# Optimization experiments

Hardware: AMD Instinct MI355X
Metric: run time of the kernel (lower is better)

## Reference

```python
import jax, jax.numpy as jnp
import numpy as np

NUM_ITERS = 15
EPSILON = 0.05
MESH_ITERS = 3


def _cost_proj(x, W1, b1, W2, b2):
    # Linear -> ReLU -> Linear
    h = jax.nn.relu(x @ W1 + b1)
    return h @ W2 + b2


def setup_inputs() -> dict:
    key = jax.random.key(0)
    ks = jax.random.split(key, 4)
    B, K, M, D = 8192, 32, 32, 256
    s = 1.0 / np.sqrt(D)
    return {
        "slots_q": jax.random.normal(ks[0], (B, K, D), dtype=jnp.float32),
        "slots_r": jax.random.normal(ks[1], (B, M, D), dtype=jnp.float32),
        "W1": (jax.random.normal(ks[2], (D, D), dtype=jnp.float32) * s),
        "b1": jnp.zeros((D,), dtype=jnp.float32),
        "W2": (jax.random.normal(ks[3], (D, D), dtype=jnp.float32) * s),
        "b2": jnp.zeros((D,), dtype=jnp.float32),
    }


def reference(slots_q, slots_r, W1, b1, W2, b2):
    q = _cost_proj(slots_q, W1, b1, W2, b2)  # [B,K,D]
    r = _cost_proj(slots_r, W1, b1, W2, b2)  # [B,M,D]
    # torch.cdist p=2: pairwise euclidean distance
    sq = (jnp.sum(q * q, -1)[:, :, None]
          + jnp.sum(r * r, -1)[:, None, :]
          - 2.0 * jnp.einsum('bkd,bmd->bkm', q, r))
    C = jnp.sqrt(jnp.clip(sq, 0.0))  # [B,K,M]
    B, K, M = C.shape
    log_K = -C / EPSILON
    log_a = jnp.zeros((B, K, 1), dtype=C.dtype)
    log_b = jnp.zeros((B, 1, M), dtype=C.dtype)
    for _ in range(NUM_ITERS):
        log_a = -jax.nn.logsumexp(log_K + log_b, axis=2, keepdims=True)
        log_b = -jax.nn.logsumexp(log_K + log_a, axis=1, keepdims=True)
    T = jnp.exp(log_K + log_a + log_b)
    for _ in range(MESH_ITERS):
        T = T ** 2
        T = T / (jnp.sum(T, axis=-1, keepdims=True) + 1e-8)
        T = T / (jnp.sum(T, axis=-2, keepdims=True) + 1e-8)
    cost = jnp.sum(T * C, axis=(-1, -2))  # [B]
    similarity = jax.nn.sigmoid(-cost)
    return similarity, T, C, cost
```

## Files before the change

kernel.cpp:

```cpp
#include <hip/hip_runtime.h>
#include <hip/hip_bf16.h>


typedef unsigned short u16;
typedef short short8 __attribute__((ext_vector_type(8)));
typedef float f32x4  __attribute__((ext_vector_type(4)));

#define MFMA(a, b, c) __builtin_amdgcn_mfma_f32_16x16x32_bf16((a), (b), (c), 0, 0, 0)

static __device__ __forceinline__ u16 f2bf(float f) {
  __hip_bfloat16 h = __float2bfloat16(f);
  return __builtin_bit_cast(u16, h);
}
static __device__ __forceinline__ float bf2f(u16 h) {
  return __uint_as_float(((unsigned)h) << 16);
}

__global__ __launch_bounds__(256) void prep_w(const float* __restrict__ W1,
                                              const float* __restrict__ W2,
                                              u16* __restrict__ ws) {
  int id = blockIdx.x * 256 + threadIdx.x;
  int mat = id >> 16;
  int e = id & 65535;
  int k = e >> 8, n = e & 255;
  float wv = (mat ? W2 : W1)[e];
  int ki = k >> 5, kl = k & 31;
  int g = kl >> 3, j = kl & 7;
  int lane = g * 16 + (n & 15);
  int ctg = n >> 4;
  ws[mat * 65536 + ((((ki * 16 + ctg) * 64 + lane) << 3) | j)] = f2bf(wv);
}

struct __align__(16) SMemA {
  u16 F[16384];
  float nrm[64];
};

static __device__ __forceinline__ void gemm_frag(const u16* __restrict__ Af,
                                                 const u16* __restrict__ wf,
                                                 int w, int lane, f32x4 acc[4][2]) {
#pragma unroll
  for (int rt = 0; rt < 4; ++rt) {
    acc[rt][0] = f32x4{0.f, 0.f, 0.f, 0.f};
    acc[rt][1] = f32x4{0.f, 0.f, 0.f, 0.f};
  }
  __builtin_amdgcn_s_setprio(1);
#pragma unroll
  for (int ki = 0; ki < 8; ++ki) {
    const u16* bp = wf + (((ki * 16 + 2 * w) * 64 + lane) << 3);
    short8 b0 = *reinterpret_cast<const short8*>(bp);
    short8 b1 = *reinterpret_cast<const short8*>(bp + 512);
    short8 a[4];
#pragma unroll
    for (int rt = 0; rt < 4; ++rt)
      a[rt] = *reinterpret_cast<const short8*>(Af + (((ki * 4 + rt) * 64 + lane) << 3));
#pragma unroll
    for (int rt = 0; rt < 4; ++rt) {
      acc[rt][0] = MFMA(a[rt], b0, acc[rt][0]);
      acc[rt][1] = MFMA(a[rt], b1, acc[rt][1]);
    }
  }
  __builtin_amdgcn_s_setprio(0);
}

__global__ __launch_bounds__(512, 6) void gemm_cdist(
    const float* __restrict__ slots_q, const float* __restrict__ slots_r,
    const float* __restrict__ b1, const float* __restrict__ b2,
    const u16* __restrict__ ws, float* __restrict__ CO) {
  __shared__ SMemA sm;
  const int tid = threadIdx.x, b = blockIdx.x;
  const int w = tid >> 6, lane = tid & 63, g = lane >> 4, ln = lane & 15;

  {
    const float* srcq = slots_q + (size_t)b * 8192;
    const float* srcr = slots_r + (size_t)b * 8192;
#pragma unroll
    for (int ii = 0; ii < 4; ++ii) {
      int s = tid + ii * 512;
      int ki = s >> 8, rt = (s >> 6) & 3, sg = (s >> 4) & 3, sln = s & 15;
      int row = rt * 16 + sln;
      const float* src = (row < 32) ? (srcq + row * 256) : (srcr + (row - 32) * 256);
      int k0 = ki * 32 + sg * 8;
      float4 v0 = *reinterpret_cast<const float4*>(src + k0);
      float4 v1 = *reinterpret_cast<const float4*>(src + k0 + 4);
      short8 o;
      o[0] = (short)f2bf(v0.x); o[1] = (short)f2bf(v0.y);
      o[2] = (short)f2bf(v0.z); o[3] = (short)f2bf(v0.w);
      o[4] = (short)f2bf(v1.x); o[5] = (short)f2bf(v1.y);
      o[6] = (short)f2bf(v1.z); o[7] = (short)f2bf(v1.w);
      *reinterpret_cast<short8*>(&sm.F[s << 3]) = o;
    }
  }
  float bv1a = b1[32 * w + ln], bv1b = b1[32 * w + 16 + ln];
  float bv2a = b2[32 * w + ln], bv2b = b2[32 * w + 16 + ln];
  __syncthreads();

  f32x4 acc[4][2];
  gemm_frag(sm.F, ws, w, lane, acc);
  __syncthreads();
#pragma unroll
  for (int ct = 0; ct < 2; ++ct) {
    float bv = ct ? bv1b : bv1a;
#pragma unroll
    for (int rt = 0; rt < 4; ++rt)
#pragma unroll
      for (int ri = 0; ri < 4; ++ri) {
        int lane2 = (2 * ct + (ln >> 3)) * 16 + 4 * g + ri;
        sm.F[(((w * 4 + rt) * 64 + lane2) << 3) | (ln & 7)] =
            f2bf(fmaxf(acc[rt][ct][ri] + bv, 0.0f));
      }
  }
  __syncthreads();

  gemm_frag(sm.F, ws + 65536, w, lane, acc);
  __syncthreads();
#pragma unroll
  for (int ct = 0; ct < 2; ++ct) {
    float bv = ct ? bv2b : bv2a;
#pragma unroll
    for (int rt = 0; rt < 4; ++rt)
#pragma unroll
      for (int ri = 0; ri < 4; ++ri) {
        int lane2 = (2 * ct + (ln >> 3)) * 16 + 4 * g + ri;
        sm.F[(((w * 4 + rt) * 64 + lane2) << 3) | (ln & 7)] =
            f2bf(acc[rt][ct][ri] + bv);
      }
  }
  __syncthreads();

  f32x4 dacc = f32x4{0.f, 0.f, 0.f, 0.f};
  if (w < 4) {
    const int mt = w >> 1, nt = w & 1;
    __builtin_amdgcn_s_setprio(1);
#pragma unroll
    for (int ki = 0; ki < 8; ++ki) {
      short8 aq = *reinterpret_cast<const short8*>(
          &sm.F[(((ki * 4 + mt) * 64 + lane) << 3)]);
      short8 br = *reinterpret_cast<const short8*>(
          &sm.F[(((ki * 4 + 2 + nt) * 64 + lane) << 3)]);
      dacc = MFMA(aq, br, dacc);
    }
    __builtin_amdgcn_s_setprio(0);
  } else {
    const int t = w - 4;
    float s = 0.f;
#pragma unroll
    for (int ki = 0; ki < 8; ++ki) {
      short8 v = *reinterpret_cast<const short8*>(
          &sm.F[(((ki * 4 + t) * 64 + lane) << 3)]);
#pragma unroll
      for (int i = 0; i < 8; ++i) {
        float f = bf2f((u16)v[i]);
        s = fmaf(f, f, s);
      }
    }
    s += __shfl_xor(s, 16);
    s += __shfl_xor(s, 32);
    if (lane < 16) sm.nrm[t * 16 + lane] = s;
  }
  __syncthreads();

  if (w < 4) {
    const int mt = w >> 1, nt = w & 1;
    float* Cp = CO + (size_t)b * 1024;
#pragma unroll
    for (int ri = 0; ri < 4; ++ri) {
      int k = mt * 16 + 4 * g + ri;
      int m = nt * 16 + ln;
      float sq = sm.nrm[k] + sm.nrm[32 + m] - 2.0f * dacc[ri];
      Cp[k * 32 + m] = sqrtf(fmaxf(sq, 0.0f));
    }
  }
}

__global__ __launch_bounds__(256, 4) void sinkhorn_mesh(
    const float* __restrict__ CO, float* __restrict__ simO,
    float* __restrict__ TO, float* __restrict__ costO, int Bn) {
  __shared__ float Wl[4][32 * 33];
  __shared__ float ABl[4][64];
  const int wv = threadIdx.x >> 6, lane = threadIdx.x & 63;
  const int p = blockIdx.x * 4 + wv;
  if (p >= Bn) return;
  const int h = lane >> 5, q = lane & 31;
  float* Wm = Wl[wv];
  float* LA = ABl[wv];
  float* LB = ABl[wv] + 32;
  const float* Cp = CO + (size_t)p * 1024;

  float lkr[16], lkc[16];
#pragma unroll
  for (int jj = 0; jj < 4; ++jj) {
    float4 v = *reinterpret_cast<const float4*>(Cp + q * 32 + h * 16 + jj * 4);
    int base = q * 33 + h * 16 + jj * 4;
    Wm[base + 0] = v.x; Wm[base + 1] = v.y; Wm[base + 2] = v.z; Wm[base + 3] = v.w;
    lkr[jj * 4 + 0] = -20.f * v.x; lkr[jj * 4 + 1] = -20.f * v.y;
    lkr[jj * 4 + 2] = -20.f * v.z; lkr[jj * 4 + 3] = -20.f * v.w;
  }
  LB[q] = 0.0f;
  __builtin_amdgcn_wave_barrier();
#pragma unroll
  for (int j = 0; j < 16; ++j) lkc[j] = -20.f * Wm[(h * 16 + j) * 33 + q];

  for (int it = 0; it < 15; ++it) {
    float v[16], mx, s;
#pragma unroll
    for (int j = 0; j < 16; ++j) v[j] = lkr[j] + LB[h * 16 + j];
    mx = v[0];
#pragma unroll
    for (int j = 1; j < 16; ++j) mx = fmaxf(mx, v[j]);
    mx = fmaxf(mx, __shfl_xor(mx, 32));
    s = 0.f;
#pragma unroll
    for (int j = 0; j < 16; ++j) s += __expf(v[j] - mx);
    s += __shfl_xor(s, 32);
    LA[q] = -(mx + __logf(s));
    __builtin_amdgcn_wave_barrier();
#pragma unroll
    for (int j = 0; j < 16; ++j) v[j] = lkc[j] + LA[h * 16 + j];
    mx = v[0];
#pragma unroll
    for (int j = 1; j < 16; ++j) mx = fmaxf(mx, v[j]);
    mx = fmaxf(mx, __shfl_xor(mx, 32));
    s = 0.f;
#pragma unroll
    for (int j = 0; j < 16; ++j) s += __expf(v[j] - mx);
    s += __shfl_xor(s, 32);
    LB[q] = -(mx + __logf(s));
    __builtin_amdgcn_wave_barrier();
  }

  float t[16];
  {
    float la = LA[q];
#pragma unroll
    for (int j = 0; j < 16; ++j) t[j] = __expf(lkr[j] + la + LB[h * 16 + j]);
  }

  for (int mi = 0; mi < 3; ++mi) {
    float s = 0.f;
#pragma unroll
    for (int j = 0; j < 16; ++j) { t[j] *= t[j]; s += t[j]; }
    s += __shfl_xor(s, 32);
    float inv = 1.0f / (s + 1e-8f);
#pragma unroll
    for (int j = 0; j < 16; ++j) Wm[q * 33 + h * 16 + j] = t[j] * inv;
    __builtin_amdgcn_wave_barrier();
#pragma unroll
    for (int j = 0; j < 16; ++j) t[j] = Wm[(h * 16 + j) * 33 + q];
    s = 0.f;
#pragma unroll
    for (int j = 0; j < 16; ++j) s += t[j];
    s += __shfl_xor(s, 32);
    inv = 1.0f / (s + 1e-8f);
#pragma unroll
    for (int j = 0; j < 16; ++j) Wm[(h * 16 + j) * 33 + q] = t[j] * inv;
    __builtin_amdgcn_wave_barrier();
#pragma unroll
    for (int j = 0; j < 16; ++j) t[j] = Wm[q * 33 + h * 16 + j];
  }

  float pp = 0.f;
#pragma unroll
  for (int j = 0; j < 16; ++j) pp = fmaf(t[j], -0.05f * lkr[j], pp);
  pp += __shfl_xor(pp, 1); pp += __shfl_xor(pp, 2); pp += __shfl_xor(pp, 4);
  pp += __shfl_xor(pp, 8); pp += __shfl_xor(pp, 16); pp += __shfl_xor(pp, 32);
  if (lane == 0) {
    costO[p] = pp;
    simO[p] = 1.0f / (1.0f + __expf(pp));
  }
#pragma unroll
  for (int jj = 0; jj < 4; ++jj) {
    float4 o;
    o.x = t[jj * 4 + 0]; o.y = t[jj * 4 + 1];
    o.z = t[jj * 4 + 2]; o.w = t[jj * 4 + 3];
    *reinterpret_cast<float4*>(TO + (size_t)p * 1024 + q * 32 + h * 16 + jj * 4) = o;
  }
}

extern "C" void kernel_launch(void* const* d_in, const int* in_sizes, int n_in,
                              void* d_out, int out_size, void* d_ws, size_t ws_size,
                              hipStream_t stream) {
  const float* slots_q = (const float*)d_in[0];
  const float* slots_r = (const float*)d_in[1];
  const float* W1 = (const float*)d_in[2];
  const float* b1 = (const float*)d_in[3];
  const float* W2 = (const float*)d_in[4];
  const float* b2 = (const float*)d_in[5];
  float* out = (float*)d_out;

  const int Bn = in_sizes[0] / 8192;
  u16* ws = (u16*)d_ws;

  prep_w<<<dim3(512), dim3(256), 0, stream>>>(W1, W2, ws);

  float* simO = out;
  float* TO = out + Bn;
  float* CO = TO + (size_t)Bn * 1024;
  float* costO = CO + (size_t)Bn * 1024;

  gemm_cdist<<<dim3(Bn), dim3(512), 0, stream>>>(slots_q, slots_r, b1, b2, ws, CO);
  sinkhorn_mesh<<<dim3((Bn + 3) / 4), dim3(256), 0, stream>>>(CO, simO, TO, costO, Bn);
}
```

Before: 264.3 us.

## Fuse Sinkhorn and mesh stage into the GEMM/cdist kernel via shared memory

```diff
diff --git a/kernel.cpp b/kernel.cpp
--- a/kernel.cpp
+++ b/kernel.cpp
@@ -63,10 +63,12 @@
   __builtin_amdgcn_s_setprio(0);
 }
 
-__global__ __launch_bounds__(512, 6) void gemm_cdist(
+__global__ __launch_bounds__(512, 8) void gemm_sink(
     const float* __restrict__ slots_q, const float* __restrict__ slots_r,
     const float* __restrict__ b1, const float* __restrict__ b2,
-    const u16* __restrict__ ws, float* __restrict__ CO) {
+    const u16* __restrict__ ws, float* __restrict__ simO,
+    float* __restrict__ TO, float* __restrict__ CO,
+    float* __restrict__ costO) {
   __shared__ SMemA sm;
   const int tid = threadIdx.x, b = blockIdx.x;
   const int w = tid >> 6, lane = tid & 63, g = lane >> 4, ln = lane & 15;
@@ -160,6 +162,8 @@
   }
   __syncthreads();
 
+  float* Cm = reinterpret_cast<float*>(sm.F);
+  float* Wm = Cm + 1056;
   if (w < 4) {
     const int mt = w >> 1, nt = w & 1;
     float* Cp = CO + (size_t)b * 1024;
@@ -168,38 +172,22 @@
       int k = mt * 16 + 4 * g + ri;
       int m = nt * 16 + ln;
       float sq = sm.nrm[k] + sm.nrm[32 + m] - 2.0f * dacc[ri];
-      Cp[k * 32 + m] = sqrtf(fmaxf(sq, 0.0f));
-    }
-  }
-}
-
-__global__ __launch_bounds__(256, 4) void sinkhorn_mesh(
-    const float* __restrict__ CO, float* __restrict__ simO,
-    float* __restrict__ TO, float* __restrict__ costO, int Bn) {
-  __shared__ float Wl[4][32 * 33];
-  __shared__ float ABl[4][64];
-  const int wv = threadIdx.x >> 6, lane = threadIdx.x & 63;
-  const int p = blockIdx.x * 4 + wv;
-  if (p >= Bn) return;
+      float c = sqrtf(fmaxf(sq, 0.0f));
+      Cp[k * 32 + m] = c;
+      Cm[k * 33 + m] = c;
+    }
+  }
+  __syncthreads();
+  if (w != 0) return;
+
   const int h = lane >> 5, q = lane & 31;
-  float* Wm = Wl[wv];
-  float* LA = ABl[wv];
-  float* LB = ABl[wv] + 32;
-  const float* Cp = CO + (size_t)p * 1024;
-
-  float lkr[16], lkc[16];
-#pragma unroll
-  for (int jj = 0; jj < 4; ++jj) {
-    float4 v = *reinterpret_cast<const float4*>(Cp + q * 32 + h * 16 + jj * 4);
-    int base = q * 33 + h * 16 + jj * 4;
-    Wm[base + 0] = v.x; Wm[base + 1] = v.y; Wm[base + 2] = v.z; Wm[base + 3] = v.w;
-    lkr[jj * 4 + 0] = -20.f * v.x; lkr[jj * 4 + 1] = -20.f * v.y;
-    lkr[jj * 4 + 2] = -20.f * v.z; lkr[jj * 4 + 3] = -20.f * v.w;
-  }
-  LB[q] = 0.0f;
+  float* LA = sm.nrm;
+  float* LB = sm.nrm + 32;
+  float lkr[16];
+#pragma unroll
+  for (int j = 0; j < 16; ++j) lkr[j] = -20.f * Cm[q * 33 + h * 16 + j];
+  if (lane < 32) LB[lane] = 0.0f;
   __builtin_amdgcn_wave_barrier();
-#pragma unroll
-  for (int j = 0; j < 16; ++j) lkc[j] = -20.f * Wm[(h * 16 + j) * 33 + q];
 
   for (int it = 0; it < 15; ++it) {
     float v[16], mx, s;
@@ -216,7 +204,8 @@
     LA[q] = -(mx + __logf(s));
     __builtin_amdgcn_wave_barrier();
 #pragma unroll
-    for (int j = 0; j < 16; ++j) v[j] = lkc[j] + LA[h * 16 + j];
+    for (int j = 0; j < 16; ++j)
+      v[j] = fmaf(-20.f, Cm[(h * 16 + j) * 33 + q], LA[h * 16 + j]);
     mx = v[0];
 #pragma unroll
     for (int j = 1; j < 16; ++j) mx = fmaxf(mx, v[j]);
@@ -265,15 +254,15 @@
   pp += __shfl_xor(pp, 1); pp += __shfl_xor(pp, 2); pp += __shfl_xor(pp, 4);
   pp += __shfl_xor(pp, 8); pp += __shfl_xor(pp, 16); pp += __shfl_xor(pp, 32);
   if (lane == 0) {
-    costO[p] = pp;
-    simO[p] = 1.0f / (1.0f + __expf(pp));
+    costO[b] = pp;
+    simO[b] = 1.0f / (1.0f + __expf(pp));
   }
 #pragma unroll
   for (int jj = 0; jj < 4; ++jj) {
     float4 o;
     o.x = t[jj * 4 + 0]; o.y = t[jj * 4 + 1];
     o.z = t[jj * 4 + 2]; o.w = t[jj * 4 + 3];
-    *reinterpret_cast<float4*>(TO + (size_t)p * 1024 + q * 32 + h * 16 + jj * 4) = o;
+    *reinterpret_cast<float4*>(TO + (size_t)b * 1024 + q * 32 + h * 16 + jj * 4) = o;
   }
 }
 
@@ -298,6 +287,6 @@
   float* CO = TO + (size_t)Bn * 1024;
   float* costO = CO + (size_t)Bn * 1024;
 
-  gemm_cdist<<<dim3(Bn), dim3(512), 0, stream>>>(slots_q, slots_r, b1, b2, ws, CO);
-  sinkhorn_mesh<<<dim3((Bn + 3) / 4), dim3(256), 0, stream>>>(CO, simO, TO, costO, Bn);
-}
+  gemm_sink<<<dim3(Bn), dim3(512), 0, stream>>>(slots_q, slots_r, b1, b2, ws,
+                                                simO, TO, CO, costO);
+}
```

After: 287.2 us. 1.09x slower.
